# Performance work log

Measured on AMD Instinct MI355X. Metric: run time of the kernel, lower is better.

Reference implementation:

```python
import jax, jax.numpy as jnp
import numpy as np
from jax import lax

DECAY = 0.1
THRESH = 0.5
LENS = 1.0
D_IN = 2 * 34 * 34  # 2312
HID = 800
NC = 10

@jax.custom_vjp
def act_fun(x):
    return (x > THRESH).astype(x.dtype)

def _act_fwd(x):
    return act_fun(x), x

def _act_bwd(x, g):
    p = jax.nn.sigmoid((x - THRESH) / LENS)
    return (g * p * (1.0 - p) / LENS,)

act_fun.defvjp(_act_fwd, _act_bwd)


def setup_inputs() -> dict:
    key = jax.random.key(0)
    ks = jax.random.split(key, 8)
    B, T = 128, 300
    inp = jax.random.uniform(ks[0], (B, 2, 34, 34, 50), dtype=jnp.float32)
    X = jnp.zeros((B, 2, 34, 34, T), dtype=jnp.float32)
    idx = jax.random.randint(ks[1], (B,), 0, T - 50)
    W1 = jax.random.normal(ks[2], (HID, D_IN), dtype=jnp.float32) * 0.02
    b1 = jnp.zeros((HID,), dtype=jnp.float32)
    W2 = jax.random.normal(ks[3], (NC, HID), dtype=jnp.float32) * 0.03
    b2 = jnp.zeros((NC,), dtype=jnp.float32)
    Wc = jax.random.uniform(ks[4], (1, HID + 4), dtype=jnp.float32)  # ctrl init U(0,1)
    bc = jax.random.uniform(ks[5], (1,), dtype=jnp.float32)
    return {"input": inp, "X": X, "idx": idx, "W1": W1, "b1": b1,
            "W2": W2, "b2": b2, "Wc": Wc, "bc": bc}


def _paste(Xi, clip_i, idx_i):
    # X[i, :, :, :, idx:idx+50] = input[i].view(2,34,34,50)
    return lax.dynamic_update_slice(Xi, clip_i, (0, 0, 0, idx_i))


def reference(input, X, idx, W1, b1, W2, b2, Wc, bc):
    B = X.shape[0]
    T = X.shape[-1]
    X = jax.vmap(_paste)(X, input, idx.astype(jnp.int32))
    xs = jnp.moveaxis(X.reshape(B, D_IN, T), -1, 0)  # [T, B, D_IN]

    t = jnp.arange(T)
    freqs = jnp.stack([
        jnp.ones(T), (t % 2 == 0).astype(jnp.float32),
        (t % 10 == 0).astype(jnp.float32), (t % 100 == 0).astype(jnp.float32),
    ], axis=1).astype(X.dtype)  # [T, 4]
    is_first = (t == 0)

    f32 = X.dtype
    carry0 = (
        jnp.zeros((B, HID), f32), jnp.zeros((B, HID), f32),   # h1_mem, h1_spike
        jnp.zeros((B, NC), f32), jnp.zeros((B, NC), f32),     # h2_mem, h2_spike
        jnp.zeros((B, 1), f32), jnp.zeros((B, 1), f32),       # c_mem, c_spike
        jnp.ones((B, 1), f32), jnp.zeros((B, NC), f32),       # bgt, h2_sumspike
    )

    def step(carry, inps):
        h1m, h1s, h2m, h2s, cm, cs, bgt, sum2 = carry
        x, fq, first = inps
        x_a = jnp.where(first, x, x * cs)
        bgt = jnp.where(cs == 1.0, bgt + 1.0, bgt)
        h1m = h1m * DECAY * (1.0 - h1s) + x_a @ W1.T + b1
        h1s = act_fun(h1m)
        h2m = h2m * DECAY * (1.0 - h2s) + h1s @ W2.T + b2
        h2s = act_fun(h2m)
        c_in = jnp.concatenate(
            [lax.stop_gradient(h1s), jnp.broadcast_to(fq, (B, 4))], axis=1)
        cm = cm * 0.1 * (1.0 - cs) + c_in @ Wc.T + bc
        cs = act_fun(cm)
        sum2 = sum2 + h2s
        return (h1m, h1s, h2m, h2s, cm, cs, bgt, sum2), None

    carry, _ = lax.scan(step, carry0, (xs, freqs, is_first))
    bgt, sum2 = carry[6], carry[7]
    rate = sum2 / bgt
    return rate, X
```

## Files before the change

kernel.cpp:

```cpp
#include <hip/hip_runtime.h>

#define D_IN 2312
#define HID  800
#define NCLS 10
#define BATCH 128
#define TSTEPS 300
#define WIN  50

#define MT 32
#define NT 64
#define BKK 16
#define NTILES_M 200
#define NTILES_N 13
#define GEMM_BLOCKS (NTILES_M * NTILES_N)
#define PASTE_BLOCKS 4096
#define TOTQ (BATCH * D_IN * (TSTEPS / 4))

__global__ __launch_bounds__(64) void fused_kernel(
    const float* __restrict__ inp,
    const float* __restrict__ W1,
    const int*   __restrict__ idx,
    float*       __restrict__ P,
    float*       __restrict__ outX)
{
  __shared__ float As[BKK][MT];
  __shared__ float Bs[BKK][NT + 4];

  int l  = threadIdx.x;
  int bx = blockIdx.x;

  if (bx < GEMM_BLOCKS) {
    int nt = bx / NTILES_M;
    int mt = bx - nt * NTILES_M;
    int m0 = mt * MT, n0 = nt * NT;

    int am = l & 31;
    int ak = l >> 5;
    int r  = m0 + am;
    int bb = r / 50, ss = r - bb * 50;
    const float* aptr = inp + (size_t)bb * (D_IN * WIN) + ss;

    int bn = l >> 4;
    int bk = l & 15;

    int lm = l >> 3;
    int ln = l & 7;
    int tm = lm * 4, tn = ln * 8;

    float aN[8], bN[16];
#pragma unroll
    for (int q = 0; q < 8; ++q) aN[q] = aptr[(ak * 8 + q) * WIN];
#pragma unroll
    for (int p = 0; p < 16; ++p) {
      int n = n0 + bn + 4 * p;
      bN[p] = (n < HID) ? W1[(size_t)n * D_IN + bk] : 0.f;
    }

    float acc[4][8] = {};

    for (int k0 = 0; k0 < D_IN; k0 += BKK) {
#pragma unroll
      for (int q = 0; q < 8; ++q) As[ak * 8 + q][am] = aN[q];
#pragma unroll
      for (int p = 0; p < 16; ++p) Bs[bk][bn + 4 * p] = bN[p];
      __syncthreads();

      int kn0 = k0 + BKK;
      if (kn0 < D_IN) {
#pragma unroll
        for (int q = 0; q < 8; ++q) {
          int kk = kn0 + ak * 8 + q;
          aN[q] = (kk < D_IN) ? aptr[kk * WIN] : 0.f;
        }
#pragma unroll
        for (int p = 0; p < 16; ++p) {
          int n  = n0 + bn + 4 * p;
          int kk = kn0 + bk;
          bN[p] = (n < HID && kk < D_IN) ? W1[(size_t)n * D_IN + kk] : 0.f;
        }
      }

#pragma unroll
      for (int kk = 0; kk < BKK; ++kk) {
        float4 A0 = *(const float4*)&As[kk][tm];
        float4 B0 = *(const float4*)&Bs[kk][tn];
        float4 B1 = *(const float4*)&Bs[kk][tn + 4];
        float av[4] = {A0.x, A0.y, A0.z, A0.w};
        float bv[8] = {B0.x, B0.y, B0.z, B0.w, B1.x, B1.y, B1.z, B1.w};
#pragma unroll
        for (int i = 0; i < 4; ++i)
#pragma unroll
          for (int j = 0; j < 8; ++j)
            acc[i][j] += av[i] * bv[j];
      }
      __syncthreads();
    }

    if (n0 + tn < HID) {
#pragma unroll
      for (int i = 0; i < 4; ++i) {
        int row = m0 + tm + i;
        *(float4*)&P[(size_t)row * HID + n0 + tn] =
            make_float4(acc[i][0], acc[i][1], acc[i][2], acc[i][3]);
        *(float4*)&P[(size_t)row * HID + n0 + tn + 4] =
            make_float4(acc[i][4], acc[i][5], acc[i][6], acc[i][7]);
      }
    }
  } else {
    int tid = (bx - GEMM_BLOCKS) * 64 + l;
    const int stride = PASTE_BLOCKS * 64;
    for (int i = tid; i < TOTQ; i += stride) {
      int q  = i % 75;
      int rd = i / 75;
      int b  = rd / D_IN;
      int d  = rd - b * D_IN;
      int ib = idx[b];
      const float* ip = inp + (size_t)b * (D_IN * WIN) + (size_t)d * WIN;
      int t0 = q * 4;
      float v[4];
#pragma unroll
      for (int e = 0; e < 4; ++e) {
        unsigned w = (unsigned)(t0 + e - ib);
        v[e] = (w < (unsigned)WIN) ? ip[w] : 0.f;
      }
      *(float4*)&outX[(size_t)rd * TSTEPS + t0] = make_float4(v[0], v[1], v[2], v[3]);
    }
  }
}

__global__ __launch_bounds__(64) void recur_kernel(
    const float* __restrict__ P,
    const float* __restrict__ W2,
    const float* __restrict__ b2,
    const float* __restrict__ Wc,
    const float* __restrict__ bc,
    const float* __restrict__ b1,
    const int*   __restrict__ idx,
    float*       __restrict__ out)
{
  __shared__ float sW2t[832][12];
  __shared__ float sWc[832];
  __shared__ unsigned long long sMask[64][13];
  __shared__ int sSteps[64];

  int L = threadIdx.x;
  int b = blockIdx.x;

#pragma unroll
  for (int c = 0; c < 10; ++c)
    for (int base = 0; base < 832; base += 64) {
      int j = base + L;
      sW2t[j][c] = (j < HID) ? W2[c * HID + j] : 0.f;
    }
  for (int base = 0; base < 832; base += 64) {
    int j = base + L;
    sWc[j] = (j < HID) ? Wc[j] : 0.f;
  }

  int myidx = idx[b];
  const float* Pb = P + (size_t)b * WIN * HID;

  float m[13], s[13], b1r[13], pn[13];
#pragma unroll
  for (int rr = 0; rr < 13; ++rr) {
    int j = L + 64 * rr;
    m[rr] = 0.f; s[rr] = 0.f;
    b1r[rr] = (j < HID) ? b1[j] : 0.f;
  }

  float h2m[10], h2s[10], sum2[10], b2r[10];
#pragma unroll
  for (int c = 0; c < 10; ++c) { h2m[c] = 0.f; h2s[c] = 0.f; sum2[c] = 0.f; b2r[c] = b2[c]; }
  float cm = 0.f, cs = 0.f, bgt = 1.f;
  float bc0 = bc[0];
  float wf0 = Wc[HID], wf1 = Wc[HID + 1], wf2 = Wc[HID + 2], wf3 = Wc[HID + 3];

  int cnt = 0;
  int tproc = 0;

  auto h2gap = [&]() {
#pragma unroll
    for (int c = 0; c < 10; ++c) {
      float v = (h2s[c] != 0.f ? 0.f : h2m[c] * 0.1f) + b2r[c];
      h2m[c] = v;
      h2s[c] = (v > 0.5f) ? 1.f : 0.f;
      sum2[c] += h2s[c];
    }
  };

  auto flush = [&]() {
    for (int u = 0; u < cnt; ++u) {
      int ts = sSteps[u];
      for (; tproc < ts; ++tproc) h2gap();
      float acc[10];
#pragma unroll
      for (int c = 0; c < 10; ++c) acc[c] = 0.f;
#pragma unroll
      for (int rr = 0; rr < 13; ++rr) {
        unsigned long long msk = sMask[u][rr];
        float f = (float)((unsigned)((msk >> L) & 1ull));
        const float4* row = (const float4*)&sW2t[L + 64 * rr][0];
        float4 r0 = row[0], r1 = row[1], r2 = row[2];
        acc[0] += f * r0.x; acc[1] += f * r0.y; acc[2] += f * r0.z; acc[3] += f * r0.w;
        acc[4] += f * r1.x; acc[5] += f * r1.y; acc[6] += f * r1.z; acc[7] += f * r1.w;
        acc[8] += f * r2.x; acc[9] += f * r2.y;
      }
#pragma unroll
      for (int c = 0; c < 10; ++c) {
        float v = acc[c];
        v += __shfl_xor(v, 1);
        v += __shfl_xor(v, 2);
        v += __shfl_xor(v, 4);
        v += __shfl_xor(v, 8);
        v += __shfl_xor(v, 16);
        v += __shfl_xor(v, 32);
        acc[c] = v;
      }
#pragma unroll
      for (int c = 0; c < 10; ++c) {
        float v = (h2s[c] != 0.f ? 0.f : h2m[c] * 0.1f) + acc[c] + b2r[c];
        h2m[c] = v;
        h2s[c] = (v > 0.5f) ? 1.f : 0.f;
        sum2[c] += h2s[c];
      }
      ++tproc;
    }
    cnt = 0;
  };

  __syncthreads();

  {
    unsigned w = (unsigned)(0 - myidx);
    if (w < (unsigned)WIN) {
      const float* Pr = Pb + (size_t)w * HID;
#pragma unroll
      for (int rr = 0; rr < 13; ++rr) { int j = L + 64 * rr; pn[rr] = (j < HID) ? Pr[j] : 0.f; }
    } else {
#pragma unroll
      for (int rr = 0; rr < 13; ++rr) pn[rr] = 0.f;
    }
  }

  for (int step = 0; step < TSTEPS; ++step) {
    float cur[13];
#pragma unroll
    for (int rr = 0; rr < 13; ++rr) cur[rr] = pn[rr];

    {
      unsigned w = (unsigned)(step + 1 - myidx);
      if (w < (unsigned)WIN) {
        const float* Pr = Pb + (size_t)w * HID;
#pragma unroll
        for (int rr = 0; rr < 13; ++rr) { int j = L + 64 * rr; pn[rr] = (j < HID) ? Pr[j] : 0.f; }
      } else {
#pragma unroll
        for (int rr = 0; rr < 13; ++rr) pn[rr] = 0.f;
      }
    }

    float gate = (step == 0) ? 1.f : cs;

    float sany = 0.f;
#pragma unroll
    for (int rr = 0; rr < 13; ++rr) {
      float mv = (s[rr] != 0.f ? 0.f : m[rr] * 0.1f) + cur[rr] * gate + b1r[rr];
      m[rr] = mv;
      s[rr] = (mv > 0.5f) ? 1.f : 0.f;
      sany += s[rr];
    }
    unsigned long long ball = __ballot(sany != 0.f);

    float ctrl = 0.f;
    if (ball) {
      float cacc = 0.f;
#pragma unroll
      for (int rr = 0; rr < 13; ++rr) cacc += s[rr] * sWc[L + 64 * rr];
      cacc += __shfl_xor(cacc, 1);
      cacc += __shfl_xor(cacc, 2);
      cacc += __shfl_xor(cacc, 4);
      cacc += __shfl_xor(cacc, 8);
      cacc += __shfl_xor(cacc, 16);
      cacc += __shfl_xor(cacc, 32);
      ctrl = cacc;

      unsigned long long mym = 0ull;
#pragma unroll
      for (int rr = 0; rr < 13; ++rr) {
        unsigned long long bl = __ballot(s[rr] != 0.f);
        if (L == rr) mym = bl;
      }
      if (L < 13) sMask[cnt][L] = mym;
      if (L == 0) sSteps[cnt] = step;
      ++cnt;
      if (cnt == 64) flush();
    }

    bgt += (cs == 1.f) ? 1.f : 0.f;
    float fq = wf0;
    if ((step & 1) == 0)   fq += wf1;
    if (step % 10 == 0)    fq += wf2;
    if (step % 100 == 0)   fq += wf3;
    float cv = (cs != 0.f ? 0.f : cm * 0.1f) + ctrl + fq + bc0;
    cm = cv;
    cs = (cv > 0.5f) ? 1.f : 0.f;
  }

  flush();
  for (; tproc < TSTEPS; ++tproc) h2gap();

  if (L == 0) {
#pragma unroll
    for (int c = 0; c < 10; ++c) out[b * NCLS + c] = sum2[c] / bgt;
  }
}

extern "C" void kernel_launch(void* const* d_in, const int* in_sizes, int n_in,
                              void* d_out, int out_size, void* d_ws, size_t ws_size,
                              hipStream_t stream) {
  const float* inp = (const float*)d_in[0];
  const int*   idx = (const int*)d_in[2];
  const float* W1  = (const float*)d_in[3];
  const float* b1  = (const float*)d_in[4];
  const float* W2  = (const float*)d_in[5];
  const float* b2  = (const float*)d_in[6];
  const float* Wc  = (const float*)d_in[7];
  const float* bc  = (const float*)d_in[8];

  float* out = (float*)d_out;
  float* P   = (float*)d_ws;

  fused_kernel<<<GEMM_BLOCKS + PASTE_BLOCKS, 64, 0, stream>>>(
      inp, W1, idx, P, out + BATCH * NCLS);

  recur_kernel<<<BATCH, 64, 0, stream>>>(P, W2, b2, Wc, bc, b1, idx, out);
}
```

Measured before the change: 1.252 ms.

## Shrink GEMM N-tile and defer layer-2 recurrence into single post-pass

The projection GEMM tile width drops from 64 to 32 columns. That gives 25 exact N tiles, removes the bounds checks, and makes more blocks with fewer accumulators per thread. The recurrent kernel now stores each spiking step's per-lane 13-bit spike mask as a ushort in shared memory for all 300 steps. It runs the layer-2 dot products and state update in one pass after the loop, replacing the periodic 64-entry ballot-based flush. It also skips the P row load when the gate is zero and drops the prefetch, which may expose load latency on the serial path.

Result: no change. 1.228 ms (-1.9%).

```diff
diff --git a/kernel.cpp b/kernel.cpp
--- a/kernel.cpp
+++ b/kernel.cpp
@@ -8,10 +8,10 @@
 #define WIN  50
 
 #define MT 32
-#define NT 64
+#define NT 32
 #define BKK 16
 #define NTILES_M 200
-#define NTILES_N 13
+#define NTILES_N 25
 #define GEMM_BLOCKS (NTILES_M * NTILES_N)
 #define PASTE_BLOCKS 4096
 #define TOTQ (BATCH * D_IN * (TSTEPS / 4))
@@ -43,26 +43,24 @@
     int bn = l >> 4;
     int bk = l & 15;
 
-    int lm = l >> 3;
-    int ln = l & 7;
-    int tm = lm * 4, tn = ln * 8;
-
-    float aN[8], bN[16];
+    int lm = l & 7;
+    int ln = l >> 3;
+    int tm = lm * 4, tn = ln * 4;
+
+    float aN[8], bN[8];
 #pragma unroll
     for (int q = 0; q < 8; ++q) aN[q] = aptr[(ak * 8 + q) * WIN];
 #pragma unroll
-    for (int p = 0; p < 16; ++p) {
-      int n = n0 + bn + 4 * p;
-      bN[p] = (n < HID) ? W1[(size_t)n * D_IN + bk] : 0.f;
-    }
-
-    float acc[4][8] = {};
+    for (int p = 0; p < 8; ++p)
+      bN[p] = W1[(size_t)(n0 + bn + 4 * p) * D_IN + bk];
+
+    float acc[4][4] = {};
 
     for (int k0 = 0; k0 < D_IN; k0 += BKK) {
 #pragma unroll
       for (int q = 0; q < 8; ++q) As[ak * 8 + q][am] = aN[q];
 #pragma unroll
-      for (int p = 0; p < 16; ++p) Bs[bk][bn + 4 * p] = bN[p];
+      for (int p = 0; p < 8; ++p) Bs[bk][bn + 4 * p] = bN[p];
       __syncthreads();
 
       int kn0 = k0 + BKK;
@@ -73,10 +71,9 @@
           aN[q] = (kk < D_IN) ? aptr[kk * WIN] : 0.f;
         }
 #pragma unroll
-        for (int p = 0; p < 16; ++p) {
-          int n  = n0 + bn + 4 * p;
+        for (int p = 0; p < 8; ++p) {
           int kk = kn0 + bk;
-          bN[p] = (n < HID && kk < D_IN) ? W1[(size_t)n * D_IN + kk] : 0.f;
+          bN[p] = (kk < D_IN) ? W1[(size_t)(n0 + bn + 4 * p) * D_IN + kk] : 0.f;
         }
       }
 
@@ -84,27 +81,22 @@
       for (int kk = 0; kk < BKK; ++kk) {
         float4 A0 = *(const float4*)&As[kk][tm];
         float4 B0 = *(const float4*)&Bs[kk][tn];
-        float4 B1 = *(const float4*)&Bs[kk][tn + 4];
         float av[4] = {A0.x, A0.y, A0.z, A0.w};
-        float bv[8] = {B0.x, B0.y, B0.z, B0.w, B1.x, B1.y, B1.z, B1.w};
+        float bv[4] = {B0.x, B0.y, B0.z, B0.w};
 #pragma unroll
         for (int i = 0; i < 4; ++i)
 #pragma unroll
-          for (int j = 0; j < 8; ++j)
+          for (int j = 0; j < 4; ++j)
             acc[i][j] += av[i] * bv[j];
       }
       __syncthreads();
     }
 
-    if (n0 + tn < HID) {
-#pragma unroll
-      for (int i = 0; i < 4; ++i) {
-        int row = m0 + tm + i;
-        *(float4*)&P[(size_t)row * HID + n0 + tn] =
-            make_float4(acc[i][0], acc[i][1], acc[i][2], acc[i][3]);
-        *(float4*)&P[(size_t)row * HID + n0 + tn + 4] =
-            make_float4(acc[i][4], acc[i][5], acc[i][6], acc[i][7]);
-      }
+#pragma unroll
+    for (int i = 0; i < 4; ++i) {
+      int row = m0 + tm + i;
+      *(float4*)&P[(size_t)row * HID + n0 + tn] =
+          make_float4(acc[i][0], acc[i][1], acc[i][2], acc[i][3]);
     }
   } else {
     int tid = (bx - GEMM_BLOCKS) * 64 + l;
@@ -138,19 +130,19 @@
     const int*   __restrict__ idx,
     float*       __restrict__ out)
 {
-  __shared__ float sW2t[832][12];
+  __shared__ float sW2row[NCLS][832];
   __shared__ float sWc[832];
-  __shared__ unsigned long long sMask[64][13];
-  __shared__ int sSteps[64];
+  __shared__ unsigned short sM[TSTEPS][64];
+  __shared__ int sSteps[TSTEPS];
 
   int L = threadIdx.x;
   int b = blockIdx.x;
 
 #pragma unroll
-  for (int c = 0; c < 10; ++c)
+  for (int c = 0; c < NCLS; ++c)
     for (int base = 0; base < 832; base += 64) {
       int j = base + L;
-      sW2t[j][c] = (j < HID) ? W2[c * HID + j] : 0.f;
+      sW2row[c][j] = (j < HID) ? W2[c * HID + j] : 0.f;
     }
   for (int base = 0; base < 832; base += 64) {
     int j = base + L;
@@ -160,122 +152,58 @@
   int myidx = idx[b];
   const float* Pb = P + (size_t)b * WIN * HID;
 
-  float m[13], s[13], b1r[13], pn[13];
+  float m[13], b1r[13];
+  unsigned smask = 0;
 #pragma unroll
   for (int rr = 0; rr < 13; ++rr) {
     int j = L + 64 * rr;
-    m[rr] = 0.f; s[rr] = 0.f;
+    m[rr] = 0.f;
     b1r[rr] = (j < HID) ? b1[j] : 0.f;
   }
 
-  float h2m[10], h2s[10], sum2[10], b2r[10];
-#pragma unroll
-  for (int c = 0; c < 10; ++c) { h2m[c] = 0.f; h2s[c] = 0.f; sum2[c] = 0.f; b2r[c] = b2[c]; }
   float cm = 0.f, cs = 0.f, bgt = 1.f;
   float bc0 = bc[0];
   float wf0 = Wc[HID], wf1 = Wc[HID + 1], wf2 = Wc[HID + 2], wf3 = Wc[HID + 3];
-
   int cnt = 0;
-  int tproc = 0;
-
-  auto h2gap = [&]() {
-#pragma unroll
-    for (int c = 0; c < 10; ++c) {
-      float v = (h2s[c] != 0.f ? 0.f : h2m[c] * 0.1f) + b2r[c];
-      h2m[c] = v;
-      h2s[c] = (v > 0.5f) ? 1.f : 0.f;
-      sum2[c] += h2s[c];
-    }
-  };
-
-  auto flush = [&]() {
-    for (int u = 0; u < cnt; ++u) {
-      int ts = sSteps[u];
-      for (; tproc < ts; ++tproc) h2gap();
-      float acc[10];
-#pragma unroll
-      for (int c = 0; c < 10; ++c) acc[c] = 0.f;
+
+  __syncthreads();
+
+  for (int step = 0; step < TSTEPS; ++step) {
+    float gate = (step == 0) ? 1.f : cs;
+    unsigned w = (unsigned)(step - myidx);
+    float cur[13];
+    if (w < (unsigned)WIN && gate != 0.f) {
+      const float* Pr = Pb + (size_t)w * HID;
 #pragma unroll
       for (int rr = 0; rr < 13; ++rr) {
-        unsigned long long msk = sMask[u][rr];
-        float f = (float)((unsigned)((msk >> L) & 1ull));
-        const float4* row = (const float4*)&sW2t[L + 64 * rr][0];
-        float4 r0 = row[0], r1 = row[1], r2 = row[2];
-        acc[0] += f * r0.x; acc[1] += f * r0.y; acc[2] += f * r0.z; acc[3] += f * r0.w;
-        acc[4] += f * r1.x; acc[5] += f * r1.y; acc[6] += f * r1.z; acc[7] += f * r1.w;
-        acc[8] += f * r2.x; acc[9] += f * r2.y;
-      }
-#pragma unroll
-      for (int c = 0; c < 10; ++c) {
-        float v = acc[c];
-        v += __shfl_xor(v, 1);
-        v += __shfl_xor(v, 2);
-        v += __shfl_xor(v, 4);
-        v += __shfl_xor(v, 8);
-        v += __shfl_xor(v, 16);
-        v += __shfl_xor(v, 32);
-        acc[c] = v;
-      }
-#pragma unroll
-      for (int c = 0; c < 10; ++c) {
-        float v = (h2s[c] != 0.f ? 0.f : h2m[c] * 0.1f) + acc[c] + b2r[c];
-        h2m[c] = v;
-        h2s[c] = (v > 0.5f) ? 1.f : 0.f;
-        sum2[c] += h2s[c];
-      }
-      ++tproc;
-    }
-    cnt = 0;
-  };
-
-  __syncthreads();
-
-  {
-    unsigned w = (unsigned)(0 - myidx);
-    if (w < (unsigned)WIN) {
-      const float* Pr = Pb + (size_t)w * HID;
-#pragma unroll
-      for (int rr = 0; rr < 13; ++rr) { int j = L + 64 * rr; pn[rr] = (j < HID) ? Pr[j] : 0.f; }
+        int j = L + 64 * rr;
+        cur[rr] = (j < HID) ? Pr[j] : 0.f;
+      }
     } else {
 #pragma unroll
-      for (int rr = 0; rr < 13; ++rr) pn[rr] = 0.f;
-    }
-  }
-
-  for (int step = 0; step < TSTEPS; ++step) {
-    float cur[13];
-#pragma unroll
-    for (int rr = 0; rr < 13; ++rr) cur[rr] = pn[rr];
-
-    {
-      unsigned w = (unsigned)(step + 1 - myidx);
-      if (w < (unsigned)WIN) {
-        const float* Pr = Pb + (size_t)w * HID;
-#pragma unroll
-        for (int rr = 0; rr < 13; ++rr) { int j = L + 64 * rr; pn[rr] = (j < HID) ? Pr[j] : 0.f; }
-      } else {
-#pragma unroll
-        for (int rr = 0; rr < 13; ++rr) pn[rr] = 0.f;
-      }
-    }
-
-    float gate = (step == 0) ? 1.f : cs;
-
-    float sany = 0.f;
+      for (int rr = 0; rr < 13; ++rr) cur[rr] = 0.f;
+    }
+
+    unsigned nmask = 0;
 #pragma unroll
     for (int rr = 0; rr < 13; ++rr) {
-      float mv = (s[rr] != 0.f ? 0.f : m[rr] * 0.1f) + cur[rr] * gate + b1r[rr];
+      float mprev = ((smask >> rr) & 1u) ? 0.f : m[rr] * 0.1f;
+      float mv = mprev + cur[rr] * gate + b1r[rr];
       m[rr] = mv;
-      s[rr] = (mv > 0.5f) ? 1.f : 0.f;
-      sany += s[rr];
-    }
-    unsigned long long ball = __ballot(sany != 0.f);
+      nmask |= (mv > 0.5f) ? (1u << rr) : 0u;
+    }
+    smask = nmask;
+
+    unsigned long long ball = __ballot(smask != 0u);
 
     float ctrl = 0.f;
     if (ball) {
       float cacc = 0.f;
 #pragma unroll
-      for (int rr = 0; rr < 13; ++rr) cacc += s[rr] * sWc[L + 64 * rr];
+      for (int rr = 0; rr < 13; ++rr) {
+        float f = (float)((smask >> rr) & 1u);
+        cacc = fmaf(f, sWc[L + 64 * rr], cacc);
+      }
       cacc += __shfl_xor(cacc, 1);
       cacc += __shfl_xor(cacc, 2);
       cacc += __shfl_xor(cacc, 4);
@@ -284,16 +212,9 @@
       cacc += __shfl_xor(cacc, 32);
       ctrl = cacc;
 
-      unsigned long long mym = 0ull;
-#pragma unroll
-      for (int rr = 0; rr < 13; ++rr) {
-        unsigned long long bl = __ballot(s[rr] != 0.f);
-        if (L == rr) mym = bl;
-      }
-      if (L < 13) sMask[cnt][L] = mym;
+      sM[cnt][L] = (unsigned short)smask;
       if (L == 0) sSteps[cnt] = step;
       ++cnt;
-      if (cnt == 64) flush();
     }
 
     bgt += (cs == 1.f) ? 1.f : 0.f;
@@ -306,12 +227,52 @@
     cs = (cv > 0.5f) ? 1.f : 0.f;
   }
 
-  flush();
-  for (; tproc < TSTEPS; ++tproc) h2gap();
+  float h2m[10], h2s[10], sum2[10], b2r[10];
+#pragma unroll
+  for (int c = 0; c < NCLS; ++c) { h2m[c] = 0.f; h2s[c] = 0.f; sum2[c] = 0.f; b2r[c] = b2[c]; }
+
+  int ptr = 0;
+  for (int t = 0; t < TSTEPS; ++t) {
+    float dot[10];
+#pragma unroll
+    for (int c = 0; c < NCLS; ++c) dot[c] = 0.f;
+
+    if (ptr < cnt && sSteps[ptr] == t) {
+      unsigned msk = (unsigned)sM[ptr][L];
+#pragma unroll
+      for (int rr = 0; rr < 13; ++rr) {
+        float f = (float)((msk >> rr) & 1u);
+        int j = L + 64 * rr;
+#pragma unroll
+        for (int c = 0; c < NCLS; ++c)
+          dot[c] = fmaf(f, sW2row[c][j], dot[c]);
+      }
+#pragma unroll
+      for (int c = 0; c < NCLS; ++c) {
+        float v = dot[c];
+        v += __shfl_xor(v, 1);
+        v += __shfl_xor(v, 2);
+        v += __shfl_xor(v, 4);
+        v += __shfl_xor(v, 8);
+        v += __shfl_xor(v, 16);
+        v += __shfl_xor(v, 32);
+        dot[c] = v;
+      }
+      ++ptr;
+    }
+
+#pragma unroll
+    for (int c = 0; c < NCLS; ++c) {
+      float v = (h2s[c] != 0.f ? 0.f : h2m[c] * 0.1f) + dot[c] + b2r[c];
+      h2m[c] = v;
+      h2s[c] = (v > 0.5f) ? 1.f : 0.f;
+      sum2[c] += h2s[c];
+    }
+  }
 
   if (L == 0) {
 #pragma unroll
-    for (int c = 0; c < 10; ++c) out[b * NCLS + c] = sum2[c] / bgt;
+    for (int c = 0; c < NCLS; ++c) out[b * NCLS + c] = sum2[c] / bgt;
   }
 }
 
```
